# Kernel optimization log

Hardware: AMD Instinct MI355X
Metric: run time of the kernel (lower is better)

Reference implementation:

```python
import jax, jax.numpy as jnp
import numpy as np

TOP_K = 8

def setup_inputs() -> dict:
    key = jax.random.key(0)
    k1, k2, k3, k4 = jax.random.split(key, 4)
    B, T, C, E = 4, 4096, 2048, 64
    x = jax.random.normal(k1, (B, T, C), dtype=jnp.float32)
    w_route = jax.random.normal(k2, (E, C), dtype=jnp.float32) * (C ** -0.5)
    w_noise = jax.random.normal(k3, (E, C), dtype=jnp.float32) * (C ** -0.5)
    noise = jax.random.normal(k4, (B, T, E), dtype=jnp.float32)
    return {"x": x, "w_route": w_route, "w_noise": w_noise, "noise": noise}

def reference(x, w_route, w_noise, noise):
    # logits = x @ W_route^T ; noise_logits = x @ W_noise^T  (bias-free Linears)
    logits = jnp.einsum('btc,ec->bte', x, w_route)
    noise_logits = jnp.einsum('btc,ec,->bte', x, w_noise, jnp.float32(1.0)) if False else jnp.einsum('btc,ec->bte', x, w_noise)
    noisy_logits = logits + noise * jax.nn.softplus(noise_logits)
    # top-k over experts, scatter into -inf tensor, then softmax
    topk_vals, indices = jax.lax.top_k(noisy_logits, TOP_K)  # (B,T,K)
    E = noisy_logits.shape[-1]
    in_topk = jax.nn.one_hot(indices, E, dtype=jnp.bool_).any(axis=-2)  # (B,T,E)
    sparse_logits = jnp.where(in_topk, noisy_logits, -jnp.inf)
    router_output = jax.nn.softmax(sparse_logits, axis=-1)
    return router_output, indices
```

## Files before the change

### kernel.cpp

```cpp
#include <hip/hip_runtime.h>
#include <math.h>


#define CDIM  2048
#define EDIM  64
#define NOUT  128
#define TOPK  8
#define NROWS 16384
#define BM    64
#define BK    32
#define KHALF 1024
#define NIT   (KHALF / BK)
#define TAU   1e-3f
#define XPS   72

typedef __attribute__((ext_vector_type(8))) short bf16x8;
typedef __attribute__((ext_vector_type(4))) float f32x4;

__device__ __forceinline__ void split8(const float4 a, const float4 b,
                                       bf16x8& h8, bf16x8& l8) {
    const float vv[8] = {a.x, a.y, a.z, a.w, b.x, b.y, b.z, b.w};
    #pragma unroll
    for (int j = 0; j < 8; ++j) {
        const __bf16 h = (__bf16)vv[j];
        const __bf16 l = (__bf16)(vv[j] - (float)h);
        h8[j] = __builtin_bit_cast(short, h);
        l8[j] = __builtin_bit_cast(short, l);
    }
}

__global__ __launch_bounds__(256)
void convert_w(const float* __restrict__ wr, const float* __restrict__ wn,
               short* __restrict__ whi, short* __restrict__ wlo) {
    const int s    = (int)blockIdx.x * 256 + (int)threadIdx.x;
    const int lane = s & 63;
    const int cg   = (s >> 6) & 7;
    const int kc   = s >> 9;
    const int col  = cg * 16 + (lane & 15);
    const int k0   = kc * 32 + (lane >> 4) * 8;
    const float* src = (col < EDIM ? wr + (size_t)col * CDIM
                                   : wn + (size_t)(col - EDIM) * CDIM) + k0;
    const float4 a = *(const float4*)src;
    const float4 b = *(const float4*)(src + 4);
    bf16x8 h8, l8; split8(a, b, h8, l8);
    *(bf16x8*)(whi + (size_t)s * 8) = h8;
    *(bf16x8*)(wlo + (size_t)s * 8) = l8;
}

__global__ __launch_bounds__(256, 2)
void router_gemm(const float* __restrict__ x,
                 const short* __restrict__ whi,
                 const short* __restrict__ wlo,
                 float* __restrict__ part)
{
    __shared__ __align__(16) short xsh[2][BM][XPS];

    const int tid  = (int)threadIdx.x;
    const int lane = tid & 63;
    const int wid  = tid >> 6;
    const int wr   = wid >> 1;
    const int wc   = wid & 1;
    const int l15  = lane & 15;
    const int q8   = (lane >> 4) * 8;
    const int q4   = (lane >> 4) * 4;
    const int half = (int)blockIdx.x & 1;
    const int row0 = ((int)blockIdx.x >> 1) * BM;

    const int srow = tid >> 2;
    const int skk  = (tid & 3) * 8;
    const float* xsrc = x + (size_t)(row0 + srow) * CDIM + half * KHALF + skk;

    f32x4 acc[2][4];
    #pragma unroll
    for (int mr = 0; mr < 2; ++mr)
        #pragma unroll
        for (int nc = 0; nc < 4; ++nc)
            acc[mr][nc] = (f32x4){0.f, 0.f, 0.f, 0.f};

    bf16x8 bh[2][4], bl[2][4];
    auto loadB = [&](int buf, int it) {
        const int base = ((half * NIT + it) * 8 + wc * 4) * 512 + lane * 8;
        #pragma unroll
        for (int nc = 0; nc < 4; ++nc) {
            bh[buf][nc] = *(const bf16x8*)(whi + base + nc * 512);
            bl[buf][nc] = *(const bf16x8*)(wlo + base + nc * 512);
        }
    };

    loadB(0, 0);
    {
        const float4 a = *(const float4*)xsrc;
        const float4 b = *(const float4*)(xsrc + 4);
        bf16x8 h8, l8; split8(a, b, h8, l8);
        *(bf16x8*)&xsh[0][srow][skk]      = h8;
        *(bf16x8*)&xsh[0][srow][32 + skk] = l8;
    }
    __syncthreads();

    #pragma unroll 2
    for (int it = 0; it < NIT; ++it) {
        const int  cur = it & 1;
        const bool pf  = (it + 1 < NIT);
        float4 pa, pb;
        if (pf) {
            loadB(cur ^ 1, it + 1);
            pa = *(const float4*)(xsrc + (it + 1) * BK);
            pb = *(const float4*)(xsrc + (it + 1) * BK + 4);
        }
        bf16x8 ah[2], al[2];
        #pragma unroll
        for (int mr = 0; mr < 2; ++mr) {
            const short* ar = &xsh[cur][wr * 32 + mr * 16 + l15][0];
            ah[mr] = *(const bf16x8*)(ar + q8);
            al[mr] = *(const bf16x8*)(ar + 32 + q8);
        }
        #pragma unroll
        for (int mr = 0; mr < 2; ++mr)
            #pragma unroll
            for (int nc = 0; nc < 4; ++nc) {
                acc[mr][nc] = __builtin_amdgcn_mfma_f32_16x16x32_bf16(ah[mr], bh[cur][nc], acc[mr][nc], 0, 0, 0);
                acc[mr][nc] = __builtin_amdgcn_mfma_f32_16x16x32_bf16(al[mr], bh[cur][nc], acc[mr][nc], 0, 0, 0);
                acc[mr][nc] = __builtin_amdgcn_mfma_f32_16x16x32_bf16(ah[mr], bl[cur][nc], acc[mr][nc], 0, 0, 0);
            }
        if (pf) {
            bf16x8 h8, l8; split8(pa, pb, h8, l8);
            *(bf16x8*)&xsh[cur ^ 1][srow][skk]      = h8;
            *(bf16x8*)&xsh[cur ^ 1][srow][32 + skk] = l8;
        }
        __syncthreads();
    }

    float* dst = part + (size_t)half * NROWS * NOUT;
    #pragma unroll
    for (int mr = 0; mr < 2; ++mr)
        #pragma unroll
        for (int nc = 0; nc < 4; ++nc)
            #pragma unroll
            for (int g = 0; g < 4; ++g)
                dst[(size_t)(row0 + wr * 32 + mr * 16 + q4 + g) * NOUT
                    + wc * 64 + nc * 16 + l15] = acc[mr][nc][g];
}

__global__ __launch_bounds__(256)
void router_epilogue(const float* __restrict__ x,
                     const float* __restrict__ w_route,
                     const float* __restrict__ w_noise,
                     const float* __restrict__ noise,
                     const float* __restrict__ part,
                     float* __restrict__ out_probs,
                     float* __restrict__ out_idx)
{
    __shared__ float vals[4][64];
    __shared__ float srt[4][64];

    const int tid  = (int)threadIdx.x;
    const int lane = tid & 63;
    const int wid  = tid >> 6;
    const int grow = (int)blockIdx.x * 4 + wid;
    const float* p0 = part;
    const float* p1 = part + (size_t)NROWS * NOUT;

    const size_t ro = (size_t)grow * NOUT;
    const float route = p0[ro + lane] + p1[ro + lane];
    const float nz    = p0[ro + EDIM + lane] + p1[ro + EDIM + lane];
    const float nv    = noise[(size_t)grow * EDIM + lane];
    const float sp = fmaxf(nz, 0.f) + log1pf(expf(-fabsf(nz)));
    const float nl = route + nv * sp;

    vals[wid][lane] = nl;
    __syncthreads();

    int cnt = 0;
    #pragma unroll
    for (int jq = 0; jq < 16; ++jq) {
        const float4 v = *(const float4*)&vals[wid][jq * 4];
        const int j0 = jq * 4;
        cnt += (v.x > nl || (v.x == nl && (j0 + 0) < lane));
        cnt += (v.y > nl || (v.y == nl && (j0 + 1) < lane));
        cnt += (v.z > nl || (v.z == nl && (j0 + 2) < lane));
        cnt += (v.w > nl || (v.w == nl && (j0 + 3) < lane));
    }
    srt[wid][cnt] = nl;
    __syncthreads();

    const float m = srt[wid][0];
    bool amb = false, flagme = false;
    float prev = m;
    #pragma unroll
    for (int t = 1; t <= TOPK; ++t) {
        const float vt = srt[wid][t];
        if (prev - vt < TAU) {
            amb = true;
            const float vb = 0.5f * (prev + vt);
            flagme = flagme || (fabsf(nl - vb) <= TAU);
        }
        prev = vt;
    }

    if (cnt < TOPK) out_idx[(size_t)grow * TOPK + cnt] = (float)lane;
    float ev = (cnt < TOPK) ? expf(nl - m) : 0.f;
    float s  = ev;
    #pragma unroll
    for (int off = 32; off >= 1; off >>= 1) s += __shfl_xor(s, off, 64);
    out_probs[(size_t)grow * EDIM + lane] = ev / s;

    if (amb) {
        unsigned long long mask = __ballot(flagme);
        double nld = (double)nl;
        const float* xr = x + (size_t)grow * CDIM;
        while (mask) {
            const int e = (int)__ffsll(mask) - 1;
            mask &= (mask - 1);
            double ar = 0.0, an = 0.0;
            const float* wrp = w_route + (size_t)e * CDIM;
            const float* wnp = w_noise + (size_t)e * CDIM;
            #pragma unroll
            for (int j = 0; j < 8; ++j) {
                const int k = (j * 64 + lane) * 4;
                const float4 xv = *(const float4*)(xr + k);
                const float4 rv = *(const float4*)(wrp + k);
                const float4 nq = *(const float4*)(wnp + k);
                ar = fma((double)xv.x, (double)rv.x, ar);
                ar = fma((double)xv.y, (double)rv.y, ar);
                ar = fma((double)xv.z, (double)rv.z, ar);
                ar = fma((double)xv.w, (double)rv.w, ar);
                an = fma((double)xv.x, (double)nq.x, an);
                an = fma((double)xv.y, (double)nq.y, an);
                an = fma((double)xv.z, (double)nq.z, an);
                an = fma((double)xv.w, (double)nq.w, an);
            }
            #pragma unroll
            for (int off = 32; off >= 1; off >>= 1) {
                ar += __shfl_xor(ar, off, 64);
                an += __shfl_xor(an, off, 64);
            }
            const double spd = fmax(an, 0.0) + log1p(exp(-fabs(an)));
            const double nve = (double)__shfl(nv, e, 64);
            const double v   = ar + nve * spd;
            if (lane == e) nld = v;
        }
        double workd = nld;
        int    rank2 = -1;
        double m2 = 0.0;
        #pragma unroll
        for (int t = 0; t < TOPK; ++t) {
            double bv = workd;
            int    bi = lane;
            #pragma unroll
            for (int off = 32; off >= 1; off >>= 1) {
                const double ov = __shfl_xor(bv, off, 64);
                const int    oi = __shfl_xor(bi, off, 64);
                if (ov > bv || (ov == bv && oi < bi)) { bv = ov; bi = oi; }
            }
            if (t == 0) m2 = bv;
            if (lane == bi) {
                rank2 = t;
                workd = -INFINITY;
                out_idx[(size_t)grow * TOPK + t] = (float)lane;
            }
        }
        float ev2 = (rank2 >= 0) ? expf((float)(nld - m2)) : 0.f;
        float s2  = ev2;
        #pragma unroll
        for (int off = 32; off >= 1; off >>= 1) s2 += __shfl_xor(s2, off, 64);
        out_probs[(size_t)grow * EDIM + lane] = ev2 / s2;
    }
}

extern "C" void kernel_launch(void* const* d_in, const int* in_sizes, int n_in,
                              void* d_out, int out_size, void* d_ws, size_t ws_size,
                              hipStream_t stream)
{
    const float* x       = (const float*)d_in[0];
    const float* w_route = (const float*)d_in[1];
    const float* w_noise = (const float*)d_in[2];
    const float* noise   = (const float*)d_in[3];

    const int n_rows = in_sizes[0] / CDIM;
    float* out_probs = (float*)d_out;
    float* out_idx   = out_probs + (size_t)n_rows * EDIM;

    short* whi  = (short*)d_ws;
    short* wlo  = whi + (size_t)NOUT * CDIM;
    float* part = (float*)((char*)d_ws + 2u * 1024u * 1024u);

    hipLaunchKernelGGL(convert_w, dim3(NOUT * CDIM / (256 * 8)), dim3(256), 0, stream,
                       w_route, w_noise, whi, wlo);
    hipLaunchKernelGGL(router_gemm, dim3((n_rows / BM) * 2), dim3(256), 0, stream,
                       x, whi, wlo, part);
    hipLaunchKernelGGL(router_epilogue, dim3(n_rows / 4), dim3(256), 0, stream,
                       x, w_route, w_noise, noise, part, out_probs, out_idx);
}
```

Baseline: 253.6 us.

## Fuse router GEMM with top-k softmax epilogue and drop split-K partials

Merges the GEMM and epilogue kernels into one. Each block now handles 32 rows over the full K dimension instead of split-K halves, stages the accumulators in shared memory, and runs top-k and softmax per row in-block. This removes the partial-sum buffer write and read and one kernel launch. In exchange the grid is smaller, each wave's MFMA tile shrinks, and the per-row epilogue is serialized with block-wide syncs, which may reduce occupancy and latency hiding.

```diff
diff --git a/kernel.cpp b/kernel.cpp
--- a/kernel.cpp
+++ b/kernel.cpp
@@ -6,13 +6,12 @@
 #define EDIM  64
 #define NOUT  128
 #define TOPK  8
-#define NROWS 16384
-#define BM    64
-#define BK    32
-#define KHALF 1024
-#define NIT   (KHALF / BK)
+#define BM    32
+#define BKS   64
+#define NSIT  (CDIM / BKS)
+#define NKC   (CDIM / 32)
 #define TAU   1e-3f
-#define XPS   72
+#define XPS   136
 
 typedef __attribute__((ext_vector_type(8))) short bf16x8;
 typedef __attribute__((ext_vector_type(4))) float f32x4;
@@ -48,12 +47,19 @@
 }
 
 __global__ __launch_bounds__(256, 2)
-void router_gemm(const float* __restrict__ x,
-                 const short* __restrict__ whi,
-                 const short* __restrict__ wlo,
-                 float* __restrict__ part)
+void router_fused(const float* __restrict__ x,
+                  const short* __restrict__ whi,
+                  const short* __restrict__ wlo,
+                  const float* __restrict__ w_route,
+                  const float* __restrict__ w_noise,
+                  const float* __restrict__ noise,
+                  float* __restrict__ out_probs,
+                  float* __restrict__ out_idx)
 {
     __shared__ __align__(16) short xsh[2][BM][XPS];
+    __shared__ __align__(16) float scr[BM][NOUT + 8];
+    __shared__ __align__(16) float vals[4][64];
+    __shared__ __align__(16) float srt[4][64];
 
     const int tid  = (int)threadIdx.x;
     const int lane = tid & 63;
@@ -63,23 +69,20 @@
     const int l15  = lane & 15;
     const int q8   = (lane >> 4) * 8;
     const int q4   = (lane >> 4) * 4;
-    const int half = (int)blockIdx.x & 1;
-    const int row0 = ((int)blockIdx.x >> 1) * BM;
-
-    const int srow = tid >> 2;
-    const int skk  = (tid & 3) * 8;
-    const float* xsrc = x + (size_t)(row0 + srow) * CDIM + half * KHALF + skk;
-
-    f32x4 acc[2][4];
+    const int row0 = (int)blockIdx.x * BM;
+
+    const int srow = tid >> 3;
+    const int skk  = (tid & 7) * 8;
+    const float* xsrc = x + (size_t)(row0 + srow) * CDIM + skk;
+
+    f32x4 acc[4];
     #pragma unroll
-    for (int mr = 0; mr < 2; ++mr)
-        #pragma unroll
-        for (int nc = 0; nc < 4; ++nc)
-            acc[mr][nc] = (f32x4){0.f, 0.f, 0.f, 0.f};
+    for (int nc = 0; nc < 4; ++nc)
+        acc[nc] = (f32x4){0.f, 0.f, 0.f, 0.f};
 
     bf16x8 bh[2][4], bl[2][4];
-    auto loadB = [&](int buf, int it) {
-        const int base = ((half * NIT + it) * 8 + wc * 4) * 512 + lane * 8;
+    auto loadB = [&](int buf, int kc) {
+        const int base = (kc * 8 + wc * 4) * 512 + lane * 8;
         #pragma unroll
         for (int nc = 0; nc < 4; ++nc) {
             bh[buf][nc] = *(const bf16x8*)(whi + base + nc * 512);
@@ -93,177 +96,169 @@
         const float4 b = *(const float4*)(xsrc + 4);
         bf16x8 h8, l8; split8(a, b, h8, l8);
         *(bf16x8*)&xsh[0][srow][skk]      = h8;
-        *(bf16x8*)&xsh[0][srow][32 + skk] = l8;
+        *(bf16x8*)&xsh[0][srow][64 + skk] = l8;
     }
     __syncthreads();
 
     #pragma unroll 2
-    for (int it = 0; it < NIT; ++it) {
-        const int  cur = it & 1;
-        const bool pf  = (it + 1 < NIT);
+    for (int sit = 0; sit < NSIT; ++sit) {
+        const int  cur = sit & 1;
+        const bool pf  = (sit + 1 < NSIT);
+        const int  g0  = sit * 2;
+
+        loadB(1, g0 + 1);
         float4 pa, pb;
         if (pf) {
-            loadB(cur ^ 1, it + 1);
-            pa = *(const float4*)(xsrc + (it + 1) * BK);
-            pb = *(const float4*)(xsrc + (it + 1) * BK + 4);
-        }
-        bf16x8 ah[2], al[2];
-        #pragma unroll
-        for (int mr = 0; mr < 2; ++mr) {
-            const short* ar = &xsh[cur][wr * 32 + mr * 16 + l15][0];
-            ah[mr] = *(const bf16x8*)(ar + q8);
-            al[mr] = *(const bf16x8*)(ar + 32 + q8);
-        }
-        #pragma unroll
-        for (int mr = 0; mr < 2; ++mr)
+            pa = *(const float4*)(xsrc + (sit + 1) * BKS);
+            pb = *(const float4*)(xsrc + (sit + 1) * BKS + 4);
+        }
+
+        const short* ar = &xsh[cur][wr * 16 + l15][0];
+        {
+            const bf16x8 ah = *(const bf16x8*)(ar + q8);
+            const bf16x8 al = *(const bf16x8*)(ar + 64 + q8);
             #pragma unroll
             for (int nc = 0; nc < 4; ++nc) {
-                acc[mr][nc] = __builtin_amdgcn_mfma_f32_16x16x32_bf16(ah[mr], bh[cur][nc], acc[mr][nc], 0, 0, 0);
-                acc[mr][nc] = __builtin_amdgcn_mfma_f32_16x16x32_bf16(al[mr], bh[cur][nc], acc[mr][nc], 0, 0, 0);
-                acc[mr][nc] = __builtin_amdgcn_mfma_f32_16x16x32_bf16(ah[mr], bl[cur][nc], acc[mr][nc], 0, 0, 0);
-            }
+                acc[nc] = __builtin_amdgcn_mfma_f32_16x16x32_bf16(ah, bh[0][nc], acc[nc], 0, 0, 0);
+                acc[nc] = __builtin_amdgcn_mfma_f32_16x16x32_bf16(al, bh[0][nc], acc[nc], 0, 0, 0);
+                acc[nc] = __builtin_amdgcn_mfma_f32_16x16x32_bf16(ah, bl[0][nc], acc[nc], 0, 0, 0);
+            }
+        }
+        if (g0 + 2 < NKC) loadB(0, g0 + 2);
+        {
+            const bf16x8 ah = *(const bf16x8*)(ar + 32 + q8);
+            const bf16x8 al = *(const bf16x8*)(ar + 96 + q8);
+            #pragma unroll
+            for (int nc = 0; nc < 4; ++nc) {
+                acc[nc] = __builtin_amdgcn_mfma_f32_16x16x32_bf16(ah, bh[1][nc], acc[nc], 0, 0, 0);
+                acc[nc] = __builtin_amdgcn_mfma_f32_16x16x32_bf16(al, bh[1][nc], acc[nc], 0, 0, 0);
+                acc[nc] = __builtin_amdgcn_mfma_f32_16x16x32_bf16(ah, bl[1][nc], acc[nc], 0, 0, 0);
+            }
+        }
         if (pf) {
             bf16x8 h8, l8; split8(pa, pb, h8, l8);
             *(bf16x8*)&xsh[cur ^ 1][srow][skk]      = h8;
-            *(bf16x8*)&xsh[cur ^ 1][srow][32 + skk] = l8;
+            *(bf16x8*)&xsh[cur ^ 1][srow][64 + skk] = l8;
         }
         __syncthreads();
     }
 
-    float* dst = part + (size_t)half * NROWS * NOUT;
     #pragma unroll
-    for (int mr = 0; mr < 2; ++mr)
-        #pragma unroll
-        for (int nc = 0; nc < 4; ++nc)
-            #pragma unroll
-            for (int g = 0; g < 4; ++g)
-                dst[(size_t)(row0 + wr * 32 + mr * 16 + q4 + g) * NOUT
-                    + wc * 64 + nc * 16 + l15] = acc[mr][nc][g];
-}
-
-__global__ __launch_bounds__(256)
-void router_epilogue(const float* __restrict__ x,
-                     const float* __restrict__ w_route,
-                     const float* __restrict__ w_noise,
-                     const float* __restrict__ noise,
-                     const float* __restrict__ part,
-                     float* __restrict__ out_probs,
-                     float* __restrict__ out_idx)
-{
-    __shared__ float vals[4][64];
-    __shared__ float srt[4][64];
-
-    const int tid  = (int)threadIdx.x;
-    const int lane = tid & 63;
-    const int wid  = tid >> 6;
-    const int grow = (int)blockIdx.x * 4 + wid;
-    const float* p0 = part;
-    const float* p1 = part + (size_t)NROWS * NOUT;
-
-    const size_t ro = (size_t)grow * NOUT;
-    const float route = p0[ro + lane] + p1[ro + lane];
-    const float nz    = p0[ro + EDIM + lane] + p1[ro + EDIM + lane];
-    const float nv    = noise[(size_t)grow * EDIM + lane];
-    const float sp = fmaxf(nz, 0.f) + log1pf(expf(-fabsf(nz)));
-    const float nl = route + nv * sp;
-
-    vals[wid][lane] = nl;
+    for (int nc = 0; nc < 4; ++nc)
+        #pragma unroll
+        for (int g = 0; g < 4; ++g)
+            scr[wr * 16 + q4 + g][wc * 64 + nc * 16 + l15] = acc[nc][g];
     __syncthreads();
 
-    int cnt = 0;
-    #pragma unroll
-    for (int jq = 0; jq < 16; ++jq) {
-        const float4 v = *(const float4*)&vals[wid][jq * 4];
-        const int j0 = jq * 4;
-        cnt += (v.x > nl || (v.x == nl && (j0 + 0) < lane));
-        cnt += (v.y > nl || (v.y == nl && (j0 + 1) < lane));
-        cnt += (v.z > nl || (v.z == nl && (j0 + 2) < lane));
-        cnt += (v.w > nl || (v.w == nl && (j0 + 3) < lane));
-    }
-    srt[wid][cnt] = nl;
-    __syncthreads();
-
-    const float m = srt[wid][0];
-    bool amb = false, flagme = false;
-    float prev = m;
-    #pragma unroll
-    for (int t = 1; t <= TOPK; ++t) {
-        const float vt = srt[wid][t];
-        if (prev - vt < TAU) {
-            amb = true;
-            const float vb = 0.5f * (prev + vt);
-            flagme = flagme || (fabsf(nl - vb) <= TAU);
-        }
-        prev = vt;
-    }
-
-    if (cnt < TOPK) out_idx[(size_t)grow * TOPK + cnt] = (float)lane;
-    float ev = (cnt < TOPK) ? expf(nl - m) : 0.f;
-    float s  = ev;
-    #pragma unroll
-    for (int off = 32; off >= 1; off >>= 1) s += __shfl_xor(s, off, 64);
-    out_probs[(size_t)grow * EDIM + lane] = ev / s;
-
-    if (amb) {
-        unsigned long long mask = __ballot(flagme);
-        double nld = (double)nl;
-        const float* xr = x + (size_t)grow * CDIM;
-        while (mask) {
-            const int e = (int)__ffsll(mask) - 1;
-            mask &= (mask - 1);
-            double ar = 0.0, an = 0.0;
-            const float* wrp = w_route + (size_t)e * CDIM;
-            const float* wnp = w_noise + (size_t)e * CDIM;
-            #pragma unroll
-            for (int j = 0; j < 8; ++j) {
-                const int k = (j * 64 + lane) * 4;
-                const float4 xv = *(const float4*)(xr + k);
-                const float4 rv = *(const float4*)(wrp + k);
-                const float4 nq = *(const float4*)(wnp + k);
-                ar = fma((double)xv.x, (double)rv.x, ar);
-                ar = fma((double)xv.y, (double)rv.y, ar);
-                ar = fma((double)xv.z, (double)rv.z, ar);
-                ar = fma((double)xv.w, (double)rv.w, ar);
-                an = fma((double)xv.x, (double)nq.x, an);
-                an = fma((double)xv.y, (double)nq.y, an);
-                an = fma((double)xv.z, (double)nq.z, an);
-                an = fma((double)xv.w, (double)nq.w, an);
-            }
-            #pragma unroll
-            for (int off = 32; off >= 1; off >>= 1) {
-                ar += __shfl_xor(ar, off, 64);
-                an += __shfl_xor(an, off, 64);
-            }
-            const double spd = fmax(an, 0.0) + log1p(exp(-fabs(an)));
-            const double nve = (double)__shfl(nv, e, 64);
-            const double v   = ar + nve * spd;
-            if (lane == e) nld = v;
-        }
-        double workd = nld;
-        int    rank2 = -1;
-        double m2 = 0.0;
-        #pragma unroll
-        for (int t = 0; t < TOPK; ++t) {
-            double bv = workd;
-            int    bi = lane;
-            #pragma unroll
-            for (int off = 32; off >= 1; off >>= 1) {
-                const double ov = __shfl_xor(bv, off, 64);
-                const int    oi = __shfl_xor(bi, off, 64);
-                if (ov > bv || (ov == bv && oi < bi)) { bv = ov; bi = oi; }
-            }
-            if (t == 0) m2 = bv;
-            if (lane == bi) {
-                rank2 = t;
-                workd = -INFINITY;
-                out_idx[(size_t)grow * TOPK + t] = (float)lane;
-            }
-        }
-        float ev2 = (rank2 >= 0) ? expf((float)(nld - m2)) : 0.f;
-        float s2  = ev2;
-        #pragma unroll
-        for (int off = 32; off >= 1; off >>= 1) s2 += __shfl_xor(s2, off, 64);
-        out_probs[(size_t)grow * EDIM + lane] = ev2 / s2;
+    #pragma unroll 1
+    for (int r8 = 0; r8 < 8; ++r8) {
+        const int row  = wid * 8 + r8;
+        const int grow = row0 + row;
+
+        const float route = scr[row][lane];
+        const float nz    = scr[row][EDIM + lane];
+        const float nv    = noise[(size_t)grow * EDIM + lane];
+        const float sp = fmaxf(nz, 0.f) + log1pf(expf(-fabsf(nz)));
+        const float nl = route + nv * sp;
+
+        vals[wid][lane] = nl;
+        __syncthreads();
+
+        int cnt = 0;
+        #pragma unroll
+        for (int jq = 0; jq < 16; ++jq) {
+            const float4 v = *(const float4*)&vals[wid][jq * 4];
+            const int j0 = jq * 4;
+            cnt += (v.x > nl || (v.x == nl && (j0 + 0) < lane));
+            cnt += (v.y > nl || (v.y == nl && (j0 + 1) < lane));
+            cnt += (v.z > nl || (v.z == nl && (j0 + 2) < lane));
+            cnt += (v.w > nl || (v.w == nl && (j0 + 3) < lane));
+        }
+        srt[wid][cnt] = nl;
+        __syncthreads();
+
+        const float m = srt[wid][0];
+        bool amb = false, flagme = false;
+        float prev = m;
+        #pragma unroll
+        for (int t = 1; t <= TOPK; ++t) {
+            const float vt = srt[wid][t];
+            if (prev - vt < TAU) {
+                amb = true;
+                const float vb = 0.5f * (prev + vt);
+                flagme = flagme || (fabsf(nl - vb) <= TAU);
+            }
+            prev = vt;
+        }
+
+        if (cnt < TOPK) out_idx[(size_t)grow * TOPK + cnt] = (float)lane;
+        float ev = (cnt < TOPK) ? expf(nl - m) : 0.f;
+        float s  = ev;
+        #pragma unroll
+        for (int off = 32; off >= 1; off >>= 1) s += __shfl_xor(s, off, 64);
+        out_probs[(size_t)grow * EDIM + lane] = ev / s;
+
+        if (amb) {
+            unsigned long long mask = __ballot(flagme);
+            double nld = (double)nl;
+            const float* xr = x + (size_t)grow * CDIM;
+            while (mask) {
+                const int e = (int)__ffsll(mask) - 1;
+                mask &= (mask - 1);
+                double ar2 = 0.0, an = 0.0;
+                const float* wrp = w_route + (size_t)e * CDIM;
+                const float* wnp = w_noise + (size_t)e * CDIM;
+                #pragma unroll
+                for (int j = 0; j < 8; ++j) {
+                    const int k = (j * 64 + lane) * 4;
+                    const float4 xv = *(const float4*)(xr + k);
+                    const float4 rv = *(const float4*)(wrp + k);
+                    const float4 nq = *(const float4*)(wnp + k);
+                    ar2 = fma((double)xv.x, (double)rv.x, ar2);
+                    ar2 = fma((double)xv.y, (double)rv.y, ar2);
+                    ar2 = fma((double)xv.z, (double)rv.z, ar2);
+                    ar2 = fma((double)xv.w, (double)rv.w, ar2);
+                    an  = fma((double)xv.x, (double)nq.x, an);
+                    an  = fma((double)xv.y, (double)nq.y, an);
+                    an  = fma((double)xv.z, (double)nq.z, an);
+                    an  = fma((double)xv.w, (double)nq.w, an);
+                }
+                #pragma unroll
+                for (int off = 32; off >= 1; off >>= 1) {
+                    ar2 += __shfl_xor(ar2, off, 64);
+                    an  += __shfl_xor(an, off, 64);
+                }
+                const double spd = fmax(an, 0.0) + log1p(exp(-fabs(an)));
+                const double nve = (double)__shfl(nv, e, 64);
+                const double v   = ar2 + nve * spd;
+                if (lane == e) nld = v;
+            }
+            double workd = nld;
+            int    rank2 = -1;
+            double m2 = 0.0;
+            #pragma unroll
+            for (int t = 0; t < TOPK; ++t) {
+                double bv = workd;
+                int    bi = lane;
+                #pragma unroll
+                for (int off = 32; off >= 1; off >>= 1) {
+                    const double ov = __shfl_xor(bv, off, 64);
+                    const int    oi = __shfl_xor(bi, off, 64);
+                    if (ov > bv || (ov == bv && oi < bi)) { bv = ov; bi = oi; }
+                }
+                if (t == 0) m2 = bv;
+                if (lane == bi) {
+                    rank2 = t;
+                    workd = -INFINITY;
+                    out_idx[(size_t)grow * TOPK + t] = (float)lane;
+                }
+            }
+            float ev2 = (rank2 >= 0) ? expf((float)(nld - m2)) : 0.f;
+            float s2  = ev2;
+            #pragma unroll
+            for (int off = 32; off >= 1; off >>= 1) s2 += __shfl_xor(s2, off, 64);
+            out_probs[(size_t)grow * EDIM + lane] = ev2 / s2;
+        }
     }
 }
 
@@ -280,14 +275,11 @@
     float* out_probs = (float*)d_out;
     float* out_idx   = out_probs + (size_t)n_rows * EDIM;
 
-    short* whi  = (short*)d_ws;
-    short* wlo  = whi + (size_t)NOUT * CDIM;
-    float* part = (float*)((char*)d_ws + 2u * 1024u * 1024u);
+    short* whi = (short*)d_ws;
+    short* wlo = whi + (size_t)NOUT * CDIM;
 
     hipLaunchKernelGGL(convert_w, dim3(NOUT * CDIM / (256 * 8)), dim3(256), 0, stream,
                        w_route, w_noise, whi, wlo);
-    hipLaunchKernelGGL(router_gemm, dim3((n_rows / BM) * 2), dim3(256), 0, stream,
-                       x, whi, wlo, part);
-    hipLaunchKernelGGL(router_epilogue, dim3(n_rows / 4), dim3(256), 0, stream,
-                       x, w_route, w_noise, noise, part, out_probs, out_idx);
-}
+    hipLaunchKernelGGL(router_fused, dim3(n_rows / BM), dim3(256), 0, stream,
+                       x, whi, wlo, w_route, w_noise, noise, out_probs, out_idx);
+}
```

Measured after the change: 298.9 us. 1.18x slower.

## Split GEMM K into four slices, prefetch x two steps ahead, lighter barriers

Applied to the files above, without the earlier changes.

Raises the K-split of the router GEMM from two to four, so the grid has twice as many blocks, each covering a quarter of the channel dimension. The epilogue now sums four partial tensors. The x prefetch moves to two iterations ahead, with register double-buffering, to hide global load latency. The full __syncthreads is replaced by an LDS-only waitcnt plus s_barrier, and the barrier after the last iteration is dropped. The trade-off is twice the partial-sum traffic to and from global memory (4×16384×128 floats written and read), and the partial buffer must still fit in the workspace.

```diff
diff --git a/kernel.cpp b/kernel.cpp
--- a/kernel.cpp
+++ b/kernel.cpp
@@ -2,17 +2,18 @@
 #include <math.h>
 
 
-#define CDIM  2048
-#define EDIM  64
-#define NOUT  128
-#define TOPK  8
-#define NROWS 16384
-#define BM    64
-#define BK    32
-#define KHALF 1024
-#define NIT   (KHALF / BK)
-#define TAU   1e-3f
-#define XPS   72
+#define CDIM   2048
+#define EDIM   64
+#define NOUT   128
+#define TOPK   8
+#define NROWS  16384
+#define BM     64
+#define BK     32
+#define KSPLIT 4
+#define KQ     (CDIM / KSPLIT)
+#define NIT    (KQ / BK)
+#define TAU    1e-3f
+#define XPS    72
 
 typedef __attribute__((ext_vector_type(8))) short bf16x8;
 typedef __attribute__((ext_vector_type(4))) float f32x4;
@@ -27,6 +28,11 @@
         h8[j] = __builtin_bit_cast(short, h);
         l8[j] = __builtin_bit_cast(short, l);
     }
+}
+
+__device__ __forceinline__ void block_sync() {
+    asm volatile("s_waitcnt lgkmcnt(0)" ::: "memory");
+    __builtin_amdgcn_s_barrier();
 }
 
 __global__ __launch_bounds__(256)
@@ -63,12 +69,12 @@
     const int l15  = lane & 15;
     const int q8   = (lane >> 4) * 8;
     const int q4   = (lane >> 4) * 4;
-    const int half = (int)blockIdx.x & 1;
-    const int row0 = ((int)blockIdx.x >> 1) * BM;
+    const int qk   = (int)blockIdx.x & (KSPLIT - 1);
+    const int row0 = ((int)blockIdx.x >> 2) * BM;
 
     const int srow = tid >> 2;
     const int skk  = (tid & 3) * 8;
-    const float* xsrc = x + (size_t)(row0 + srow) * CDIM + half * KHALF + skk;
+    const float* xsrc = x + (size_t)(row0 + srow) * CDIM + qk * KQ + skk;
 
     f32x4 acc[2][4];
     #pragma unroll
@@ -79,7 +85,7 @@
 
     bf16x8 bh[2][4], bl[2][4];
     auto loadB = [&](int buf, int it) {
-        const int base = ((half * NIT + it) * 8 + wc * 4) * 512 + lane * 8;
+        const int base = ((qk * NIT + it) * 8 + wc * 4) * 512 + lane * 8;
         #pragma unroll
         for (int nc = 0; nc < 4; ++nc) {
             bh[buf][nc] = *(const bf16x8*)(whi + base + nc * 512);
@@ -95,17 +101,18 @@
         *(bf16x8*)&xsh[0][srow][skk]      = h8;
         *(bf16x8*)&xsh[0][srow][32 + skk] = l8;
     }
-    __syncthreads();
+    float4 pfa[2], pfb[2];
+    pfa[1] = *(const float4*)(xsrc + BK);
+    pfb[1] = *(const float4*)(xsrc + BK + 4);
+    block_sync();
 
     #pragma unroll 2
     for (int it = 0; it < NIT; ++it) {
-        const int  cur = it & 1;
-        const bool pf  = (it + 1 < NIT);
-        float4 pa, pb;
-        if (pf) {
-            loadB(cur ^ 1, it + 1);
-            pa = *(const float4*)(xsrc + (it + 1) * BK);
-            pb = *(const float4*)(xsrc + (it + 1) * BK + 4);
+        const int cur = it & 1;
+        if (it + 1 < NIT) loadB(cur ^ 1, it + 1);
+        if (it + 2 < NIT) {
+            pfa[cur] = *(const float4*)(xsrc + (it + 2) * BK);
+            pfb[cur] = *(const float4*)(xsrc + (it + 2) * BK + 4);
         }
         bf16x8 ah[2], al[2];
         #pragma unroll
@@ -122,15 +129,15 @@
                 acc[mr][nc] = __builtin_amdgcn_mfma_f32_16x16x32_bf16(al[mr], bh[cur][nc], acc[mr][nc], 0, 0, 0);
                 acc[mr][nc] = __builtin_amdgcn_mfma_f32_16x16x32_bf16(ah[mr], bl[cur][nc], acc[mr][nc], 0, 0, 0);
             }
-        if (pf) {
-            bf16x8 h8, l8; split8(pa, pb, h8, l8);
+        if (it + 1 < NIT) {
+            bf16x8 h8, l8; split8(pfa[cur ^ 1], pfb[cur ^ 1], h8, l8);
             *(bf16x8*)&xsh[cur ^ 1][srow][skk]      = h8;
             *(bf16x8*)&xsh[cur ^ 1][srow][32 + skk] = l8;
-        }
-        __syncthreads();
-    }
-
-    float* dst = part + (size_t)half * NROWS * NOUT;
+            block_sync();
+        }
+    }
+
+    float* dst = part + (size_t)qk * NROWS * NOUT;
     #pragma unroll
     for (int mr = 0; mr < 2; ++mr)
         #pragma unroll
@@ -159,10 +166,14 @@
     const int grow = (int)blockIdx.x * 4 + wid;
     const float* p0 = part;
     const float* p1 = part + (size_t)NROWS * NOUT;
+    const float* p2 = part + (size_t)2 * NROWS * NOUT;
+    const float* p3 = part + (size_t)3 * NROWS * NOUT;
 
     const size_t ro = (size_t)grow * NOUT;
-    const float route = p0[ro + lane] + p1[ro + lane];
-    const float nz    = p0[ro + EDIM + lane] + p1[ro + EDIM + lane];
+    const float route = (p0[ro + lane] + p1[ro + lane])
+                      + (p2[ro + lane] + p3[ro + lane]);
+    const float nz    = (p0[ro + EDIM + lane] + p1[ro + EDIM + lane])
+                      + (p2[ro + EDIM + lane] + p3[ro + EDIM + lane]);
     const float nv    = noise[(size_t)grow * EDIM + lane];
     const float sp = fmaxf(nz, 0.f) + log1pf(expf(-fabsf(nz)));
     const float nl = route + nv * sp;
@@ -286,7 +297,7 @@
 
     hipLaunchKernelGGL(convert_w, dim3(NOUT * CDIM / (256 * 8)), dim3(256), 0, stream,
                        w_route, w_noise, whi, wlo);
-    hipLaunchKernelGGL(router_gemm, dim3((n_rows / BM) * 2), dim3(256), 0, stream,
+    hipLaunchKernelGGL(router_gemm, dim3((n_rows / BM) * KSPLIT), dim3(256), 0, stream,
                        x, whi, wlo, part);
     hipLaunchKernelGGL(router_epilogue, dim3(n_rows / 4), dim3(256), 0, stream,
                        x, w_route, w_noise, noise, part, out_probs, out_idx);
```

New measurement: 249.2 us. No clear change (-1.8%).
